# Kernel optimization log

Measured on AMD Instinct MI355X. Metric: run time of the kernel, lower is better.

Reference implementation:

```python
import jax, jax.numpy as jnp
import numpy as np

INPUT_SIZE = 512
HIDDEN_SIZE = 1024
BATCH = 16384


def setup_inputs() -> dict:
    key = jax.random.key(0)
    ks = jax.random.split(key, 11)
    s_x = 1.0 / np.sqrt(INPUT_SIZE)
    s_h = 1.0 / np.sqrt(HIDDEN_SIZE)
    inp = {
        "x": jax.random.normal(ks[0], (BATCH, INPUT_SIZE), dtype=jnp.float32),
        "hidden": jax.random.normal(ks[1], (BATCH, HIDDEN_SIZE), dtype=jnp.float32),
        # Linear weights stored as (in, out) for x @ W
        "Wxr": jax.random.uniform(ks[2], (INPUT_SIZE, HIDDEN_SIZE), jnp.float32, -s_x, s_x),
        "bxr": jax.random.uniform(ks[3], (HIDDEN_SIZE,), jnp.float32, -s_x, s_x),
        "Whr": jax.random.uniform(ks[4], (HIDDEN_SIZE, HIDDEN_SIZE), jnp.float32, -s_h, s_h),
        "Wxz": jax.random.uniform(ks[5], (INPUT_SIZE, HIDDEN_SIZE), jnp.float32, -s_x, s_x),
        "bxz": jax.random.uniform(ks[6], (HIDDEN_SIZE,), jnp.float32, -s_x, s_x),
        "Whz": jax.random.uniform(ks[7], (HIDDEN_SIZE, HIDDEN_SIZE), jnp.float32, -s_h, s_h),
        "Wxh": jax.random.uniform(ks[8], (INPUT_SIZE, HIDDEN_SIZE), jnp.float32, -s_x, s_x),
        "bxh": jax.random.uniform(ks[9], (HIDDEN_SIZE,), jnp.float32, -s_x, s_x),
        "Whh": jax.random.uniform(ks[10], (HIDDEN_SIZE, HIDDEN_SIZE), jnp.float32, -s_h, s_h),
    }
    return inp


def reference(x, hidden, Wxr, bxr, Whr, Wxz, bxz, Whz, Wxh, bxh, Whh):
    # GRU cell, single timestep.
    r = jax.nn.sigmoid(x @ Wxr + bxr + hidden @ Whr)          # reset gate (B,H)
    z = jax.nn.sigmoid(x @ Wxz + bxz + hidden @ Whz)          # update gate (B,H)
    h_cand = jnp.tanh(x @ Wxh + bxh + (r * hidden) @ Whh)     # candidate (B,H)
    return z * hidden + (1.0 - z) * h_cand
```

## Files before the change

### kernel.cpp

```cpp
#include <hip/hip_runtime.h>

typedef unsigned short u16;
typedef unsigned int u32;
typedef __bf16 bf16x8 __attribute__((ext_vector_type(8)));
typedef float f32x4 __attribute__((ext_vector_type(4)));

#define B_ROWS 16384
#define K1 1536

__device__ __forceinline__ u16 f2bf(float f) {
  u32 u = __float_as_uint(f);
  u = (u + 0x7fffu + ((u >> 16) & 1u)) >> 16;
  return (u16)u;
}
__device__ __forceinline__ float bf2f(u16 b) {
  return __uint_as_float(((u32)b) << 16);
}
__device__ __forceinline__ void gload_lds16(const void* g, void* l) {
  __builtin_amdgcn_global_load_lds((const __attribute__((address_space(1))) void*)g,
                                   (__attribute__((address_space(3))) void*)l,
                                   16, 0, 0);
}

__global__ void cvt_xh(const float* __restrict__ x, const float* __restrict__ h,
                       u16* __restrict__ xh) {
  const int iv = blockIdx.x * 256 + threadIdx.x;
  const int row = iv / 384;
  const int col = (iv - row * 384) * 4;
  const float* src = (col < 512) ? x + (size_t)row * 512 + col
                                 : h + (size_t)row * 1024 + (col - 512);
  float4 v = *(const float4*)src;
  u32 a = (u32)f2bf(v.x) | ((u32)f2bf(v.y) << 16);
  u32 b = (u32)f2bf(v.z) | ((u32)f2bf(v.w) << 16);
  *(uint2*)(xh + (size_t)row * 1536 + col) = make_uint2(a, b);
}

__global__ void transpose_cvt6(const float* __restrict__ Wxr, const float* __restrict__ Whr,
                               const float* __restrict__ Wxz, const float* __restrict__ Whz,
                               const float* __restrict__ Wxh, const float* __restrict__ Whh,
                               u16* __restrict__ W1t, u16* __restrict__ W2t) {
  __shared__ float tile[32][33];
  const int z = blockIdx.z;
  const float* W;
  u16* T;
  int Ks, koff, roff;
  switch (z) {
    case 0:  W = Wxr; T = W1t; Ks = 512;  koff = 0;   roff = 0;    break;
    case 1:  W = Whr; T = W1t; Ks = 1024; koff = 512; roff = 0;    break;
    case 2:  W = Wxz; T = W1t; Ks = 512;  koff = 0;   roff = 1024; break;
    case 3:  W = Whz; T = W1t; Ks = 1024; koff = 512; roff = 1024; break;
    case 4:  W = Wxh; T = W2t; Ks = 512;  koff = 0;   roff = 0;    break;
    default: W = Whh; T = W2t; Ks = 1024; koff = 512; roff = 0;    break;
  }
  const int bx = blockIdx.x, by = blockIdx.y;
  if (by * 32 >= Ks) return;
  const int tx = threadIdx.x, ty = threadIdx.y;
#pragma unroll
  for (int r = 0; r < 32; r += 8)
    tile[ty + r][tx] = W[(size_t)(by * 32 + ty + r) * 1024 + bx * 32 + tx];
  __syncthreads();
#pragma unroll
  for (int r = 0; r < 32; r += 8)
    T[(size_t)(roff + bx * 32 + ty + r) * K1 + koff + by * 32 + tx] = f2bf(tile[tx][ty + r]);
}

struct Src {
  const u16 *a0, *a1, *b0, *b1;
  int sa0, sa1, sb0, sb1, tsplit;
};

__device__ __forceinline__ const u16* gsrc(const u16* p0, const u16* p1, int s0, int s1,
                                           int tsplit, int t, int grow) {
  return (t < tsplit) ? p0 + (size_t)grow * s0 + t * 64
                      : p1 + (size_t)grow * s1 + (t - tsplit) * 64;
}

__device__ __forceinline__ void stage_half(const u16* p0, const u16* p1, int s0, int s1,
                                           int tsplit, int t, int rowbase, int h,
                                           char* matB, int c, int tid, int kswz) {
  char* lds = matB + c * 32768 + h * 16384 + ((tid >> 6) << 10);
  const int r = tid >> 3;
  const u16* g0 = gsrc(p0, p1, s0, s1, tsplit, t, rowbase + h * 128 + r) + kswz;
  const u16* g1 = gsrc(p0, p1, s0, s1, tsplit, t, rowbase + h * 128 + 64 + r) + kswz;
  gload_lds16(g0, lds);
  gload_lds16(g1, lds + 8192);
}

#define STAGE_A(t_, c_, h_) \
  stage_half(S.a0, S.a1, S.sa0, S.sa1, S.tsplit, (t_), brow, (h_), AsB, (c_), tid, kswz)
#define STAGE_B(t_, c_, h_) \
  stage_half(S.b0, S.b1, S.sb0, S.sb1, S.tsplit, (t_), bcol, (h_), BsB, (c_), tid, kswz)

__device__ __forceinline__ void gemm256(const Src& S, int nt, int brow, int bcol,
                                        u16* AsU, u16* BsU, f32x4 acc[8][4]) {
  const int tid = threadIdx.x;
  const int l = tid & 63;
  const int wid = tid >> 6;
  const int wr = wid >> 2, wc = wid & 3;
  const int lr = l & 15, kq = l >> 4;
  const int swzB = (lr & 7) * 16;
  const int kswz = ((tid & 7) ^ ((tid >> 3) & 7)) * 8;
  char* AsB = (char*)AsU;
  char* BsB = (char*)BsU;
  const int colK0 = (kq * 16) ^ swzB;
  const int colK1 = (64 + kq * 16) ^ swzB;
  int aRow[8], bRow[4];
#pragma unroll
  for (int m = 0; m < 8; ++m) aRow[m] = (wr * 128 + m * 16 + lr) * 128;
#pragma unroll
  for (int n = 0; n < 4; ++n) bRow[n] = (wc * 64 + n * 16 + lr) * 128;

  STAGE_A(0, 0, 0);
  STAGE_A(0, 0, 1);
  STAGE_B(0, 0, 0);
  STAGE_B(0, 0, 1);
  if (1 < nt) STAGE_A(1, 1, 0);
  asm volatile("s_waitcnt vmcnt(2)" ::: "memory");
  __builtin_amdgcn_s_barrier();
  asm volatile("" ::: "memory");

  for (int t = 0; t < nt; ++t) {
    const int c = t & 1;
    const int cb = c << 15;
    bf16x8 a[4][2], b[4][2];
#pragma unroll
    for (int m = 0; m < 4; ++m) {
      a[m][0] = *(const bf16x8*)(AsB + cb + aRow[m] + colK0);
      a[m][1] = *(const bf16x8*)(AsB + cb + aRow[m] + colK1);
    }
#pragma unroll
    for (int n = 0; n < 2; ++n) {
      b[n][0] = *(const bf16x8*)(BsB + cb + bRow[n] + colK0);
      b[n][1] = *(const bf16x8*)(BsB + cb + bRow[n] + colK1);
    }
    if (t + 1 < nt) STAGE_A(t + 1, c ^ 1, 1);
    __builtin_amdgcn_s_barrier();
    asm volatile("s_waitcnt lgkmcnt(0)" ::: "memory");
    __builtin_amdgcn_sched_barrier(0);
    __builtin_amdgcn_s_setprio(1);
#pragma unroll
    for (int kk = 0; kk < 2; ++kk)
#pragma unroll
      for (int m = 0; m < 4; ++m)
#pragma unroll
        for (int n = 0; n < 2; ++n)
          acc[m][n] = __builtin_amdgcn_mfma_f32_16x16x32_bf16(a[m][kk], b[n][kk], acc[m][n], 0, 0, 0);
    __builtin_amdgcn_s_setprio(0);
    __builtin_amdgcn_s_barrier();
    asm volatile("" ::: "memory");
#pragma unroll
    for (int n = 2; n < 4; ++n) {
      b[n][0] = *(const bf16x8*)(BsB + cb + bRow[n] + colK0);
      b[n][1] = *(const bf16x8*)(BsB + cb + bRow[n] + colK1);
    }
    if (t + 1 < nt) STAGE_B(t + 1, c ^ 1, 0);
    __builtin_amdgcn_s_barrier();
    asm volatile("s_waitcnt lgkmcnt(0)" ::: "memory");
    __builtin_amdgcn_sched_barrier(0);
    __builtin_amdgcn_s_setprio(1);
#pragma unroll
    for (int kk = 0; kk < 2; ++kk)
#pragma unroll
      for (int m = 0; m < 4; ++m)
#pragma unroll
        for (int n = 2; n < 4; ++n)
          acc[m][n] = __builtin_amdgcn_mfma_f32_16x16x32_bf16(a[m][kk], b[n][kk], acc[m][n], 0, 0, 0);
    __builtin_amdgcn_s_setprio(0);
    __builtin_amdgcn_s_barrier();
    asm volatile("" ::: "memory");
#pragma unroll
    for (int m = 0; m < 4; ++m) {
      a[m][0] = *(const bf16x8*)(AsB + cb + aRow[m + 4] + colK0);
      a[m][1] = *(const bf16x8*)(AsB + cb + aRow[m + 4] + colK1);
    }
    if (t + 1 < nt) STAGE_B(t + 1, c ^ 1, 1);
    __builtin_amdgcn_s_barrier();
    asm volatile("s_waitcnt lgkmcnt(0)" ::: "memory");
    __builtin_amdgcn_sched_barrier(0);
    __builtin_amdgcn_s_setprio(1);
#pragma unroll
    for (int kk = 0; kk < 2; ++kk)
#pragma unroll
      for (int m = 0; m < 4; ++m)
#pragma unroll
        for (int n = 2; n < 4; ++n)
          acc[m + 4][n] = __builtin_amdgcn_mfma_f32_16x16x32_bf16(a[m][kk], b[n][kk], acc[m + 4][n], 0, 0, 0);
    __builtin_amdgcn_s_setprio(0);
    __builtin_amdgcn_s_barrier();
    asm volatile("" ::: "memory");
    if (t + 2 < nt) STAGE_A(t + 2, c, 0);
    __builtin_amdgcn_s_barrier();
    __builtin_amdgcn_s_setprio(1);
#pragma unroll
    for (int kk = 0; kk < 2; ++kk)
#pragma unroll
      for (int m = 0; m < 4; ++m)
#pragma unroll
        for (int n = 0; n < 2; ++n)
          acc[m + 4][n] = __builtin_amdgcn_mfma_f32_16x16x32_bf16(a[m][kk], b[n][kk], acc[m + 4][n], 0, 0, 0);
    __builtin_amdgcn_s_setprio(0);
    if (t + 2 < nt) { asm volatile("s_waitcnt vmcnt(2)" ::: "memory"); }
    else            { asm volatile("s_waitcnt vmcnt(0)" ::: "memory"); }
    __builtin_amdgcn_s_barrier();
    asm volatile("" ::: "memory");
  }
}

__global__ __launch_bounds__(512, 2) void gru_gemm1(
    const u16* __restrict__ xh, const u16* __restrict__ W1t,
    const float* __restrict__ bxr, const float* __restrict__ bxz,
    u16* __restrict__ rhb, u16* __restrict__ zb) {
  __shared__ __align__(16) u16 As[2 * 256 * 64];
  __shared__ __align__(16) u16 Bs[2 * 256 * 64];
  const int orig = blockIdx.x;
  const int slot = orig >> 3;
  const int mt = (orig & 7) + 8 * (slot >> 3);
  const int jt = slot & 7;
  const int brow = mt * 256;
  const int jcol = jt * 256;

  Src S;
  S.a0 = xh;  S.sa0 = K1; S.a1 = xh + 512;  S.sa1 = K1;
  S.b0 = W1t; S.sb0 = K1; S.b1 = W1t + 512; S.sb1 = K1;
  S.tsplit = 8;

  f32x4 acc[8][4] = {};
  gemm256(S, 24, brow, jcol, As, Bs, acc);

  const int l = threadIdx.x & 63;
  const int wid = threadIdx.x >> 6;
  const int wr = wid >> 2, wc = wid & 3;
  const int colb = jcol + wc * 64 + (l & 15);
  const int rowb = brow + wr * 128 + (l >> 4) * 4;
  if (jt < 4) {
#pragma unroll
    for (int n = 0; n < 4; ++n) {
      const int col = colb + n * 16;
      const float bias = bxr[col];
#pragma unroll
      for (int m = 0; m < 8; ++m)
#pragma unroll
        for (int j = 0; j < 4; ++j) {
          const int row = rowb + m * 16 + j;
          const float rg = 1.f / (1.f + __expf(-(acc[m][n][j] + bias)));
          const float hv = bf2f(xh[(size_t)row * K1 + 512 + col]);
          rhb[(size_t)row * 1024 + col] = f2bf(rg * hv);
        }
    }
  } else {
#pragma unroll
    for (int n = 0; n < 4; ++n) {
      const int col = colb + n * 16 - 1024;
      const float bias = bxz[col];
#pragma unroll
      for (int m = 0; m < 8; ++m)
#pragma unroll
        for (int j = 0; j < 4; ++j) {
          const int row = rowb + m * 16 + j;
          const float zg = 1.f / (1.f + __expf(-(acc[m][n][j] + bias)));
          zb[(size_t)row * 1024 + col] = f2bf(zg);
        }
    }
  }
}

__global__ __launch_bounds__(512, 2) void gru_gemm2(
    const u16* __restrict__ xh, const u16* __restrict__ rhb,
    const u16* __restrict__ W2t, const float* __restrict__ bxh,
    const u16* __restrict__ zb, const float* __restrict__ hidden,
    float* __restrict__ out) {
  __shared__ __align__(16) u16 As[2 * 256 * 64];
  __shared__ __align__(16) u16 Bs[2 * 256 * 64];
  const int orig = blockIdx.x;
  const int slot = orig >> 3;
  const int mt = (orig & 7) + 8 * (slot >> 2);
  const int jt = slot & 3;
  const int brow = mt * 256;
  const int jcol = jt * 256;

  Src S;
  S.a0 = xh;  S.sa0 = K1; S.a1 = rhb;       S.sa1 = 1024;
  S.b0 = W2t; S.sb0 = K1; S.b1 = W2t + 512; S.sb1 = K1;
  S.tsplit = 8;

  f32x4 acc[8][4] = {};
  gemm256(S, 24, brow, jcol, As, Bs, acc);

  const int l = threadIdx.x & 63;
  const int wid = threadIdx.x >> 6;
  const int wr = wid >> 2, wc = wid & 3;
  const int colb = jcol + wc * 64 + (l & 15);
  const int rowb = brow + wr * 128 + (l >> 4) * 4;
#pragma unroll
  for (int n = 0; n < 4; ++n) {
    const int col = colb + n * 16;
    const float bias = bxh[col];
#pragma unroll
    for (int m = 0; m < 8; ++m)
#pragma unroll
      for (int j = 0; j < 4; ++j) {
        const int row = rowb + m * 16 + j;
        const size_t idx = (size_t)row * 1024 + col;
        const float e = __expf(2.f * (acc[m][n][j] + bias));
        const float hc = 1.f - 2.f / (e + 1.f);
        const float z = bf2f(zb[idx]);
        const float h = hidden[idx];
        out[idx] = z * h + (1.f - z) * hc;
      }
  }
}

extern "C" void kernel_launch(void* const* d_in, const int* in_sizes, int n_in,
                              void* d_out, int out_size, void* d_ws, size_t ws_size,
                              hipStream_t stream) {
  const float* x      = (const float*)d_in[0];
  const float* hidden = (const float*)d_in[1];
  const float* Wxr = (const float*)d_in[2];
  const float* bxr = (const float*)d_in[3];
  const float* Whr = (const float*)d_in[4];
  const float* Wxz = (const float*)d_in[5];
  const float* bxz = (const float*)d_in[6];
  const float* Whz = (const float*)d_in[7];
  const float* Wxh = (const float*)d_in[8];
  const float* bxh = (const float*)d_in[9];
  const float* Whh = (const float*)d_in[10];
  float* out = (float*)d_out;
  (void)in_sizes; (void)n_in; (void)out_size; (void)ws_size;

  char* p = (char*)d_ws;
  u16* xh  = (u16*)p; p += (size_t)B_ROWS * K1 * 2;
  u16* W1t = (u16*)p; p += (size_t)2048 * K1 * 2;
  u16* W2t = (u16*)p; p += (size_t)1024 * K1 * 2;
  u16* rhb = (u16*)p; p += (size_t)B_ROWS * 1024 * 2;
  u16* zb  = (u16*)p; p += (size_t)B_ROWS * 1024 * 2;

  cvt_xh<<<B_ROWS * 384 / 256, 256, 0, stream>>>(x, hidden, xh);
  transpose_cvt6<<<dim3(32, 32, 6), dim3(32, 8), 0, stream>>>(
      Wxr, Whr, Wxz, Whz, Wxh, Whh, W1t, W2t);

  gru_gemm1<<<512, 512, 0, stream>>>(xh, W1t, bxr, bxz, rhb, zb);
  gru_gemm2<<<256, 512, 0, stream>>>(xh, rhb, W2t, bxh, zb, hidden, out);
}
```

Baseline: 292.6 us.

## Replace pipelined 256x256 GEMM with simple single-buffered 128x128 tiles

Swaps the hand-scheduled, double-buffered 256x256x64 GEMM core with 512 threads for a plain 128x128x32 tile, 256 threads and a single LDS buffer synchronized by two __syncthreads per k-step. The launch grid grows fourfold and the epilogue indexing is adjusted to the smaller tiles. The intent is more resident blocks and simpler code, but it gives up load/compute overlap and per-block data reuse, so global and LDS traffic per flop increase.

New measurement: 327.3 us. 1.12x slower.

```diff
diff --git a/kernel.cpp b/kernel.cpp
--- a/kernel.cpp
+++ b/kernel.cpp
@@ -69,176 +69,88 @@
   int sa0, sa1, sb0, sb1, tsplit;
 };
 
-__device__ __forceinline__ const u16* gsrc(const u16* p0, const u16* p1, int s0, int s1,
-                                           int tsplit, int t, int grow) {
-  return (t < tsplit) ? p0 + (size_t)grow * s0 + t * 64
-                      : p1 + (size_t)grow * s1 + (t - tsplit) * 64;
-}
-
-__device__ __forceinline__ void stage_half(const u16* p0, const u16* p1, int s0, int s1,
-                                           int tsplit, int t, int rowbase, int h,
-                                           char* matB, int c, int tid, int kswz) {
-  char* lds = matB + c * 32768 + h * 16384 + ((tid >> 6) << 10);
-  const int r = tid >> 3;
-  const u16* g0 = gsrc(p0, p1, s0, s1, tsplit, t, rowbase + h * 128 + r) + kswz;
-  const u16* g1 = gsrc(p0, p1, s0, s1, tsplit, t, rowbase + h * 128 + 64 + r) + kswz;
-  gload_lds16(g0, lds);
-  gload_lds16(g1, lds + 8192);
-}
-
-#define STAGE_A(t_, c_, h_) \
-  stage_half(S.a0, S.a1, S.sa0, S.sa1, S.tsplit, (t_), brow, (h_), AsB, (c_), tid, kswz)
-#define STAGE_B(t_, c_, h_) \
-  stage_half(S.b0, S.b1, S.sb0, S.sb1, S.tsplit, (t_), bcol, (h_), BsB, (c_), tid, kswz)
-
-__device__ __forceinline__ void gemm256(const Src& S, int nt, int brow, int bcol,
-                                        u16* AsU, u16* BsU, f32x4 acc[8][4]) {
+__device__ __forceinline__ const u16* gsrc32(const u16* p0, const u16* p1, int s0, int s1,
+                                             int tsplit, int t, int grow) {
+  return (t < tsplit) ? p0 + (size_t)grow * s0 + t * 32
+                      : p1 + (size_t)grow * s1 + (t - tsplit) * 32;
+}
+
+__device__ __forceinline__ void gemm128(const Src& S, int nt, int brow, int bcol,
+                                        u16* AsU, u16* BsU, f32x4 acc[4][4]) {
   const int tid = threadIdx.x;
   const int l = tid & 63;
-  const int wid = tid >> 6;
-  const int wr = wid >> 2, wc = wid & 3;
-  const int lr = l & 15, kq = l >> 4;
-  const int swzB = (lr & 7) * 16;
-  const int kswz = ((tid & 7) ^ ((tid >> 3) & 7)) * 8;
+  const int w = tid >> 6;
+  const int wr = w >> 1, wc = w & 1;
+  const int swz = ((l & 3) ^ ((l >> 2) & 3) ^ ((l >> 4) & 3));
+  const int sr = l >> 2;
+  const int klE = swz * 8;
+  const int swz16 = swz * 16;
   char* AsB = (char*)AsU;
   char* BsB = (char*)BsU;
-  const int colK0 = (kq * 16) ^ swzB;
-  const int colK1 = (64 + kq * 16) ^ swzB;
-  int aRow[8], bRow[4];
-#pragma unroll
-  for (int m = 0; m < 8; ++m) aRow[m] = (wr * 128 + m * 16 + lr) * 128;
-#pragma unroll
-  for (int n = 0; n < 4; ++n) bRow[n] = (wc * 64 + n * 16 + lr) * 128;
-
-  STAGE_A(0, 0, 0);
-  STAGE_A(0, 0, 1);
-  STAGE_B(0, 0, 0);
-  STAGE_B(0, 0, 1);
-  if (1 < nt) STAGE_A(1, 1, 0);
-  asm volatile("s_waitcnt vmcnt(2)" ::: "memory");
-  __builtin_amdgcn_s_barrier();
-  asm volatile("" ::: "memory");
+  const int rA0 = brow + w * 16 + sr;
+  const int rA1 = brow + (w + 4) * 16 + sr;
+  const int nB0 = bcol + w * 16 + sr;
+  const int nB1 = bcol + (w + 4) * 16 + sr;
+  int aRow[4], bRow[4];
+#pragma unroll
+  for (int m = 0; m < 4; ++m) aRow[m] = (wr * 64 + m * 16 + (l & 15)) * 64;
+#pragma unroll
+  for (int n = 0; n < 4; ++n) bRow[n] = (wc * 64 + n * 16 + (l & 15)) * 64;
 
   for (int t = 0; t < nt; ++t) {
-    const int c = t & 1;
-    const int cb = c << 15;
-    bf16x8 a[4][2], b[4][2];
-#pragma unroll
-    for (int m = 0; m < 4; ++m) {
-      a[m][0] = *(const bf16x8*)(AsB + cb + aRow[m] + colK0);
-      a[m][1] = *(const bf16x8*)(AsB + cb + aRow[m] + colK1);
-    }
-#pragma unroll
-    for (int n = 0; n < 2; ++n) {
-      b[n][0] = *(const bf16x8*)(BsB + cb + bRow[n] + colK0);
-      b[n][1] = *(const bf16x8*)(BsB + cb + bRow[n] + colK1);
-    }
-    if (t + 1 < nt) STAGE_A(t + 1, c ^ 1, 1);
-    __builtin_amdgcn_s_barrier();
-    asm volatile("s_waitcnt lgkmcnt(0)" ::: "memory");
-    __builtin_amdgcn_sched_barrier(0);
-    __builtin_amdgcn_s_setprio(1);
-#pragma unroll
-    for (int kk = 0; kk < 2; ++kk)
-#pragma unroll
-      for (int m = 0; m < 4; ++m)
-#pragma unroll
-        for (int n = 0; n < 2; ++n)
-          acc[m][n] = __builtin_amdgcn_mfma_f32_16x16x32_bf16(a[m][kk], b[n][kk], acc[m][n], 0, 0, 0);
-    __builtin_amdgcn_s_setprio(0);
-    __builtin_amdgcn_s_barrier();
-    asm volatile("" ::: "memory");
-#pragma unroll
-    for (int n = 2; n < 4; ++n) {
-      b[n][0] = *(const bf16x8*)(BsB + cb + bRow[n] + colK0);
-      b[n][1] = *(const bf16x8*)(BsB + cb + bRow[n] + colK1);
-    }
-    if (t + 1 < nt) STAGE_B(t + 1, c ^ 1, 0);
-    __builtin_amdgcn_s_barrier();
-    asm volatile("s_waitcnt lgkmcnt(0)" ::: "memory");
-    __builtin_amdgcn_sched_barrier(0);
-    __builtin_amdgcn_s_setprio(1);
-#pragma unroll
-    for (int kk = 0; kk < 2; ++kk)
-#pragma unroll
-      for (int m = 0; m < 4; ++m)
-#pragma unroll
-        for (int n = 2; n < 4; ++n)
-          acc[m][n] = __builtin_amdgcn_mfma_f32_16x16x32_bf16(a[m][kk], b[n][kk], acc[m][n], 0, 0, 0);
-    __builtin_amdgcn_s_setprio(0);
-    __builtin_amdgcn_s_barrier();
-    asm volatile("" ::: "memory");
-#pragma unroll
-    for (int m = 0; m < 4; ++m) {
-      a[m][0] = *(const bf16x8*)(AsB + cb + aRow[m + 4] + colK0);
-      a[m][1] = *(const bf16x8*)(AsB + cb + aRow[m + 4] + colK1);
-    }
-    if (t + 1 < nt) STAGE_B(t + 1, c ^ 1, 1);
-    __builtin_amdgcn_s_barrier();
-    asm volatile("s_waitcnt lgkmcnt(0)" ::: "memory");
-    __builtin_amdgcn_sched_barrier(0);
-    __builtin_amdgcn_s_setprio(1);
-#pragma unroll
-    for (int kk = 0; kk < 2; ++kk)
-#pragma unroll
-      for (int m = 0; m < 4; ++m)
-#pragma unroll
-        for (int n = 2; n < 4; ++n)
-          acc[m + 4][n] = __builtin_amdgcn_mfma_f32_16x16x32_bf16(a[m][kk], b[n][kk], acc[m + 4][n], 0, 0, 0);
-    __builtin_amdgcn_s_setprio(0);
-    __builtin_amdgcn_s_barrier();
-    asm volatile("" ::: "memory");
-    if (t + 2 < nt) STAGE_A(t + 2, c, 0);
-    __builtin_amdgcn_s_barrier();
-    __builtin_amdgcn_s_setprio(1);
-#pragma unroll
-    for (int kk = 0; kk < 2; ++kk)
-#pragma unroll
-      for (int m = 0; m < 4; ++m)
-#pragma unroll
-        for (int n = 0; n < 2; ++n)
-          acc[m + 4][n] = __builtin_amdgcn_mfma_f32_16x16x32_bf16(a[m][kk], b[n][kk], acc[m + 4][n], 0, 0, 0);
-    __builtin_amdgcn_s_setprio(0);
-    if (t + 2 < nt) { asm volatile("s_waitcnt vmcnt(2)" ::: "memory"); }
-    else            { asm volatile("s_waitcnt vmcnt(0)" ::: "memory"); }
-    __builtin_amdgcn_s_barrier();
-    asm volatile("" ::: "memory");
-  }
-}
-
-__global__ __launch_bounds__(512, 2) void gru_gemm1(
+    gload_lds16(gsrc32(S.a0, S.a1, S.sa0, S.sa1, S.tsplit, t, rA0) + klE, AsB + w * 1024);
+    gload_lds16(gsrc32(S.a0, S.a1, S.sa0, S.sa1, S.tsplit, t, rA1) + klE, AsB + (w + 4) * 1024);
+    gload_lds16(gsrc32(S.b0, S.b1, S.sb0, S.sb1, S.tsplit, t, nB0) + klE, BsB + w * 1024);
+    gload_lds16(gsrc32(S.b0, S.b1, S.sb0, S.sb1, S.tsplit, t, nB1) + klE, BsB + (w + 4) * 1024);
+    __syncthreads();
+
+    bf16x8 af[4], bfv[4];
+#pragma unroll
+    for (int m = 0; m < 4; ++m) af[m] = *(const bf16x8*)(AsB + aRow[m] + swz16);
+#pragma unroll
+    for (int n = 0; n < 4; ++n) bfv[n] = *(const bf16x8*)(BsB + bRow[n] + swz16);
+#pragma unroll
+    for (int m = 0; m < 4; ++m)
+#pragma unroll
+      for (int n = 0; n < 4; ++n)
+        acc[m][n] = __builtin_amdgcn_mfma_f32_16x16x32_bf16(af[m], bfv[n], acc[m][n], 0, 0, 0);
+    __syncthreads();
+  }
+}
+
+__global__ __launch_bounds__(256, 3) void gru_gemm1(
     const u16* __restrict__ xh, const u16* __restrict__ W1t,
     const float* __restrict__ bxr, const float* __restrict__ bxz,
     u16* __restrict__ rhb, u16* __restrict__ zb) {
-  __shared__ __align__(16) u16 As[2 * 256 * 64];
-  __shared__ __align__(16) u16 Bs[2 * 256 * 64];
+  __shared__ __align__(16) u16 As[128 * 32];
+  __shared__ __align__(16) u16 Bs[128 * 32];
   const int orig = blockIdx.x;
   const int slot = orig >> 3;
-  const int mt = (orig & 7) + 8 * (slot >> 3);
-  const int jt = slot & 7;
-  const int brow = mt * 256;
-  const int jcol = jt * 256;
+  const int jt = slot & 15;
+  const int mt = (orig & 7) + 8 * (slot >> 4);
+  const int brow = mt * 128;
+  const int bcol = jt * 128;
 
   Src S;
   S.a0 = xh;  S.sa0 = K1; S.a1 = xh + 512;  S.sa1 = K1;
   S.b0 = W1t; S.sb0 = K1; S.b1 = W1t + 512; S.sb1 = K1;
-  S.tsplit = 8;
-
-  f32x4 acc[8][4] = {};
-  gemm256(S, 24, brow, jcol, As, Bs, acc);
+  S.tsplit = 16;
+
+  f32x4 acc[4][4] = {};
+  gemm128(S, 48, brow, bcol, As, Bs, acc);
 
   const int l = threadIdx.x & 63;
-  const int wid = threadIdx.x >> 6;
-  const int wr = wid >> 2, wc = wid & 3;
-  const int colb = jcol + wc * 64 + (l & 15);
-  const int rowb = brow + wr * 128 + (l >> 4) * 4;
-  if (jt < 4) {
+  const int w = threadIdx.x >> 6;
+  const int wr = w >> 1, wc = w & 1;
+  const int colb = (jt & 7) * 128 + wc * 64 + (l & 15);
+  const int rowb = brow + wr * 64 + (l >> 4) * 4;
+  if (jt < 8) {
 #pragma unroll
     for (int n = 0; n < 4; ++n) {
       const int col = colb + n * 16;
       const float bias = bxr[col];
 #pragma unroll
-      for (int m = 0; m < 8; ++m)
+      for (int m = 0; m < 4; ++m)
 #pragma unroll
         for (int j = 0; j < 4; ++j) {
           const int row = rowb + m * 16 + j;
@@ -250,10 +162,10 @@
   } else {
 #pragma unroll
     for (int n = 0; n < 4; ++n) {
-      const int col = colb + n * 16 - 1024;
+      const int col = colb + n * 16;
       const float bias = bxz[col];
 #pragma unroll
-      for (int m = 0; m < 8; ++m)
+      for (int m = 0; m < 4; ++m)
 #pragma unroll
         for (int j = 0; j < 4; ++j) {
           const int row = rowb + m * 16 + j;
@@ -264,39 +176,39 @@
   }
 }
 
-__global__ __launch_bounds__(512, 2) void gru_gemm2(
+__global__ __launch_bounds__(256, 3) void gru_gemm2(
     const u16* __restrict__ xh, const u16* __restrict__ rhb,
     const u16* __restrict__ W2t, const float* __restrict__ bxh,
     const u16* __restrict__ zb, const float* __restrict__ hidden,
     float* __restrict__ out) {
-  __shared__ __align__(16) u16 As[2 * 256 * 64];
-  __shared__ __align__(16) u16 Bs[2 * 256 * 64];
+  __shared__ __align__(16) u16 As[128 * 32];
+  __shared__ __align__(16) u16 Bs[128 * 32];
   const int orig = blockIdx.x;
   const int slot = orig >> 3;
-  const int mt = (orig & 7) + 8 * (slot >> 2);
-  const int jt = slot & 3;
-  const int brow = mt * 256;
-  const int jcol = jt * 256;
+  const int jt = slot & 7;
+  const int mt = (orig & 7) + 8 * (slot >> 3);
+  const int brow = mt * 128;
+  const int bcol = jt * 128;
 
   Src S;
   S.a0 = xh;  S.sa0 = K1; S.a1 = rhb;       S.sa1 = 1024;
   S.b0 = W2t; S.sb0 = K1; S.b1 = W2t + 512; S.sb1 = K1;
-  S.tsplit = 8;
-
-  f32x4 acc[8][4] = {};
-  gemm256(S, 24, brow, jcol, As, Bs, acc);
+  S.tsplit = 16;
+
+  f32x4 acc[4][4] = {};
+  gemm128(S, 48, brow, bcol, As, Bs, acc);
 
   const int l = threadIdx.x & 63;
-  const int wid = threadIdx.x >> 6;
-  const int wr = wid >> 2, wc = wid & 3;
-  const int colb = jcol + wc * 64 + (l & 15);
-  const int rowb = brow + wr * 128 + (l >> 4) * 4;
+  const int w = threadIdx.x >> 6;
+  const int wr = w >> 1, wc = w & 1;
+  const int colb = bcol + wc * 64 + (l & 15);
+  const int rowb = brow + wr * 64 + (l >> 4) * 4;
 #pragma unroll
   for (int n = 0; n < 4; ++n) {
     const int col = colb + n * 16;
     const float bias = bxh[col];
 #pragma unroll
-    for (int m = 0; m < 8; ++m)
+    for (int m = 0; m < 4; ++m)
 #pragma unroll
       for (int j = 0; j < 4; ++j) {
         const int row = rowb + m * 16 + j;
@@ -338,6 +250,6 @@
   transpose_cvt6<<<dim3(32, 32, 6), dim3(32, 8), 0, stream>>>(
       Wxr, Whr, Wxz, Whz, Wxh, Whh, W1t, W2t);
 
-  gru_gemm1<<<512, 512, 0, stream>>>(xh, W1t, bxr, bxz, rhb, zb);
-  gru_gemm2<<<256, 512, 0, stream>>>(xh, rhb, W2t, bxh, zb, hidden, out);
-}
+  gru_gemm1<<<2048, 256, 0, stream>>>(xh, W1t, bxr, bxz, rhb, zb);
+  gru_gemm2<<<1024, 256, 0, stream>>>(xh, rhb, W2t, bxh, zb, hidden, out);
+}
```
